# Performance work log

Measured on AMD Instinct MI355X. Metric: run time of the kernel, lower is better.

## Reference

```python
import jax, jax.numpy as jnp
import numpy as np

B, H, S, D = 1, 8, 4096, 64


def setup_inputs() -> dict:
    key = jax.random.key(0)
    kq, kk, kv = jax.random.split(key, 3)
    Q = jax.random.normal(kq, (B, H, S, D), dtype=jnp.float32)
    K = jax.random.normal(kk, (B, H, S, D), dtype=jnp.float32)
    V = jax.random.normal(kv, (B, H, S, D), dtype=jnp.float32)
    # causal mask: 1 where attention allowed, 0 where blocked (matches masked_fill(mask==0, -inf))
    mask = jnp.tril(jnp.ones((S, S), dtype=jnp.int32))[None, None, :, :]
    return {"Q": Q, "K": K, "V": V, "mask": mask}


def reference(Q, K, V, mask):
    d_k = Q.shape[-1]
    scale = 1.0 / jnp.sqrt(jnp.asarray(d_k, Q.dtype))
    # [B,H,S,S] attention scores
    attn_score = jnp.einsum("bhqd,bhkd->bhqk", Q, K) * scale
    neg_inf = jnp.asarray(-jnp.inf, attn_score.dtype)
    attn_score = jnp.where(mask == 0, neg_inf, attn_score)
    attn_weight = jax.nn.softmax(attn_score, axis=-1)
    attn_output = jnp.einsum("bhqk,bhkd->bhqd", attn_weight, V)
    return attn_output
```

## Files before the change

### kernel.cpp

```cpp
#include <hip/hip_runtime.h>

#define S_LEN 4096
#define NHEAD 8
#define DDIM  64
#define NT    64
#define TILE_BYTES 8192
#define WS_NEEDED (2ull * NHEAD * NT * TILE_BYTES)

typedef __attribute__((ext_vector_type(4))) float f32x4;
typedef __attribute__((ext_vector_type(2))) float f32x2;
typedef __attribute__((ext_vector_type(8))) short bf16x8;

__device__ __forceinline__ unsigned cvt_pk(float lo, float hi) {
  unsigned r;
  asm("v_cvt_pk_bf16_f32 %0, %1, %2" : "=v"(r) : "v"(lo), "v"(hi));
  return r;
}
__device__ __forceinline__ float ex2(float x) {
  float r;
  asm("v_exp_f32 %0, %1" : "=v"(r) : "v"(x));
  return r;
}
__device__ __forceinline__ unsigned short f2bf(float f) {
  unsigned u = __float_as_uint(f);
  return (unsigned short)((u + 0x7fffu + ((u >> 16) & 1u)) >> 16);
}
__device__ __forceinline__ unsigned pk2(float a, float b) {
  return (unsigned)f2bf(a) | ((unsigned)f2bf(b) << 16);
}

__global__ __launch_bounds__(256)
void prepass(const float* __restrict__ K, const float* __restrict__ V,
             char* __restrict__ wsK, char* __restrict__ wsV) {
  const int bid = blockIdx.x;
  const int h = bid & 7, t = bid >> 3;
  const int tid = threadIdx.x;
  const size_t base = ((size_t)h * S_LEN + t * 64) * DDIM;
  char* ck = wsK + (size_t)(h * NT + t) * TILE_BYTES;
  char* cv = wsV + (size_t)(h * NT + t) * TILE_BYTES;
  {
    const int key = tid >> 2;
    const int fn = key >> 4, lq = key & 15;
#pragma unroll
    for (int p = 0; p < 2; ++p) {
      const int du = (tid & 3) + p * 4;
      const int kk = du >> 2, g = du & 3;
      const float* src = K + base + (size_t)key * DDIM + du * 8;
      f32x4 a = *(const f32x4*)src;
      f32x4 b = *(const f32x4*)(src + 4);
      uint4 u = {cvt_pk(a[0], a[1]), cvt_pk(a[2], a[3]),
                 cvt_pk(b[0], b[1]), cvt_pk(b[2], b[3])};
      *(uint4*)(ck + kk * 4096 + fn * 1024 + g * 256 + lq * 16) = u;
    }
  }
  {
    const int kgrp = tid >> 5;
    const int d0 = (tid & 31) * 2;
    const int kk = kgrp >> 2, g = kgrp & 3;
    float va[8], vb[8];
#pragma unroll
    for (int jj = 0; jj < 8; ++jj) {
      f32x2 x = *(const f32x2*)(V + base + (size_t)(kgrp * 8 + jj) * DDIM + d0);
      va[jj] = x[0]; vb[jj] = x[1];
    }
    uint4 ua = {cvt_pk(va[0], va[1]), cvt_pk(va[2], va[3]),
                cvt_pk(va[4], va[5]), cvt_pk(va[6], va[7])};
    uint4 ub = {cvt_pk(vb[0], vb[1]), cvt_pk(vb[2], vb[3]),
                cvt_pk(vb[4], vb[5]), cvt_pk(vb[6], vb[7])};
    const int fm0 = d0 >> 4, lq0 = d0 & 15;
    const int fm1 = (d0 + 1) >> 4, lq1 = (d0 + 1) & 15;
    *(uint4*)(cv + kk * 4096 + fm0 * 1024 + g * 256 + lq0 * 16) = ua;
    *(uint4*)(cv + kk * 4096 + fm1 * 1024 + g * 256 + lq1 * 16) = ub;
  }
}

__global__ __launch_bounds__(256)
void attn_fwd13(const float* __restrict__ Q, const char* __restrict__ wsK,
                const char* __restrict__ wsV, float* __restrict__ O) {
  __shared__ __align__(16) char pool[25344];

  const int tid = threadIdx.x, wave = tid >> 6, lane = tid & 63;
  const int g = lane >> 4, lq = lane & 15;
  const int bid = blockIdx.x, h = bid & 7, i = bid >> 3;
  const int qc = 127 - i;
  const int jd = qc >> 1;
  const int qbase = qc * 32;
  const int n = (jd >= wave) ? ((jd - wave) >> 2) + 1 : 0;

  const char* tK = wsK + (size_t)h * NT * TILE_BYTES;
  const char* tV = wsV + (size_t)h * NT * TILE_BYTES;
  const int foff = lane * 16;

  const float qsc = 0.125f * 1.44269504088896340736f;
  bf16x8 qf[2][2];
#pragma unroll
  for (int qh = 0; qh < 2; ++qh) {
    const float* qp = Q + ((size_t)h * S_LEN + qbase + qh * 16 + lq) * DDIM + g * 8;
#pragma unroll
    for (int kk = 0; kk < 2; ++kk) {
      f32x4 a = *(const f32x4*)(qp + kk * 32);
      f32x4 b = *(const f32x4*)(qp + kk * 32 + 4);
      uint4 u = {cvt_pk(a[0] * qsc, a[1] * qsc), cvt_pk(a[2] * qsc, a[3] * qsc),
                 cvt_pk(b[0] * qsc, b[1] * qsc), cvt_pk(b[2] * qsc, b[3] * qsc)};
      qf[qh][kk] = __builtin_bit_cast(bf16x8, u);
    }
  }

  f32x4 of0[4], of1[4];
#pragma unroll
  for (int fm = 0; fm < 4; ++fm) { of0[fm] = (f32x4){0,0,0,0}; of1[fm] = (f32x4){0,0,0,0}; }
  float l0 = 0.f, l1 = 0.f;

  char* pbase = pool + wave * 4608;
  const int prow = lq * 72;

  bf16x8 kf[4][2], vf[4][2];
  f32x4 s0[4], s1[4];

  if (n > 0) {
    const char* pk = tK + (size_t)wave * TILE_BYTES + foff;
    const char* pv = tV + (size_t)wave * TILE_BYTES + foff;
#pragma unroll
    for (int fn = 0; fn < 4; ++fn)
#pragma unroll
      for (int kk = 0; kk < 2; ++kk) {
        kf[fn][kk] = *(const bf16x8*)(pk + kk * 4096 + fn * 1024);
        vf[fn][kk] = *(const bf16x8*)(pv + kk * 4096 + fn * 1024);
      }
#pragma unroll
    for (int fn = 0; fn < 4; ++fn) {
      f32x4 a = (f32x4){0,0,0,0}, b = (f32x4){0,0,0,0};
      a = __builtin_amdgcn_mfma_f32_16x16x32_bf16(kf[fn][0], qf[0][0], a, 0, 0, 0);
      a = __builtin_amdgcn_mfma_f32_16x16x32_bf16(kf[fn][1], qf[0][1], a, 0, 0, 0);
      b = __builtin_amdgcn_mfma_f32_16x16x32_bf16(kf[fn][0], qf[1][0], b, 0, 0, 0);
      b = __builtin_amdgcn_mfma_f32_16x16x32_bf16(kf[fn][1], qf[1][1], b, 0, 0, 0);
      s0[fn] = a; s1[fn] = b;
    }
    if (n > 1) {
      const char* pk2 = tK + (size_t)(wave + 4) * TILE_BYTES + foff;
#pragma unroll
      for (int fn = 0; fn < 4; ++fn)
#pragma unroll
        for (int kk = 0; kk < 2; ++kk)
          kf[fn][kk] = *(const bf16x8*)(pk2 + kk * 4096 + fn * 1024);
    }
  }

  int j = wave;
  for (int it = 0; it < n; ++it, j += 4) {

    if (j == jd) {
      const int koff = qbase - jd * 64;
#pragma unroll
      for (int fn = 0; fn < 4; ++fn)
#pragma unroll
        for (int rr = 0; rr < 4; ++rr) {
          const int key = fn * 16 + g * 4 + rr;
          if (key > koff + lq)      s0[fn][rr] = -__builtin_inff();
          if (key > koff + 16 + lq) s1[fn][rr] = -__builtin_inff();
        }
    }

    float rs0 = 0.f, rs1 = 0.f;
#pragma unroll
    for (int fn = 0; fn < 4; ++fn) {
      float a00 = ex2(s0[fn][0]), a01 = ex2(s0[fn][1]);
      float a02 = ex2(s0[fn][2]), a03 = ex2(s0[fn][3]);
      float a10 = ex2(s1[fn][0]), a11 = ex2(s1[fn][1]);
      float a12 = ex2(s1[fn][2]), a13 = ex2(s1[fn][3]);
      rs0 += (a00 + a01) + (a02 + a03);
      rs1 += (a10 + a11) + (a12 + a13);
      const int kk = fn >> 1;
      const int boff = ((fn & 1) * 2 + (g >> 1)) * 16 + (g & 1) * 8;
      unsigned long long w0 = (unsigned long long)cvt_pk(a00, a01)
                            | ((unsigned long long)cvt_pk(a02, a03) << 32);
      unsigned long long w1 = (unsigned long long)cvt_pk(a10, a11)
                            | ((unsigned long long)cvt_pk(a12, a13) << 32);
      *(unsigned long long*)(pbase + (kk * 2 + 0) * 1152 + prow + boff) = w0;
      *(unsigned long long*)(pbase + (kk * 2 + 1) * 1152 + prow + boff) = w1;
    }
    l0 += rs0; l1 += rs1;

    if (it + 1 < n) {
#pragma unroll
      for (int fn = 0; fn < 4; ++fn) {
        f32x4 a = (f32x4){0,0,0,0}, b = (f32x4){0,0,0,0};
        a = __builtin_amdgcn_mfma_f32_16x16x32_bf16(kf[fn][0], qf[0][0], a, 0, 0, 0);
        a = __builtin_amdgcn_mfma_f32_16x16x32_bf16(kf[fn][1], qf[0][1], a, 0, 0, 0);
        b = __builtin_amdgcn_mfma_f32_16x16x32_bf16(kf[fn][0], qf[1][0], b, 0, 0, 0);
        b = __builtin_amdgcn_mfma_f32_16x16x32_bf16(kf[fn][1], qf[1][1], b, 0, 0, 0);
        s0[fn] = a; s1[fn] = b;
      }
    }

    asm volatile("s_waitcnt lgkmcnt(0)" ::: "memory");

#pragma unroll
    for (int kk = 0; kk < 2; ++kk) {
      bf16x8 p0 = *(const bf16x8*)(pbase + (kk * 2 + 0) * 1152 + prow + g * 16);
      bf16x8 p1 = *(const bf16x8*)(pbase + (kk * 2 + 1) * 1152 + prow + g * 16);
#pragma unroll
      for (int fm = 0; fm < 4; ++fm) {
        of0[fm] = __builtin_amdgcn_mfma_f32_16x16x32_bf16(vf[fm][kk], p0, of0[fm], 0, 0, 0);
        of1[fm] = __builtin_amdgcn_mfma_f32_16x16x32_bf16(vf[fm][kk], p1, of1[fm], 0, 0, 0);
      }
    }

    if (it + 1 < n) {
      const char* pv = tV + (size_t)(j + 4) * TILE_BYTES + foff;
#pragma unroll
      for (int fm = 0; fm < 4; ++fm)
#pragma unroll
        for (int kk = 0; kk < 2; ++kk)
          vf[fm][kk] = *(const bf16x8*)(pv + kk * 4096 + fm * 1024);
      if (it + 2 < n) {
        const char* pk = tK + (size_t)(j + 8) * TILE_BYTES + foff;
#pragma unroll
        for (int fn = 0; fn < 4; ++fn)
#pragma unroll
          for (int kk = 0; kk < 2; ++kk)
            kf[fn][kk] = *(const bf16x8*)(pk + kk * 4096 + fn * 1024);
      }
    }
  }

  l0 += __shfl_xor(l0, 16); l0 += __shfl_xor(l0, 32);
  l1 += __shfl_xor(l1, 16); l1 += __shfl_xor(l1, 32);

  __syncthreads();
  if (wave < 3) {
    char* mb = pool + wave * 8192;
#pragma unroll
    for (int fm = 0; fm < 4; ++fm) {
      *(f32x4*)(mb + (fm * 2 + 0) * 1024 + g * 256 + lq * 16) = of0[fm];
      *(f32x4*)(mb + (fm * 2 + 1) * 1024 + g * 256 + lq * 16) = of1[fm];
    }
    if (g == 0) {
      f32x4 v = {l0, l1, 0.f, 0.f};
      *(f32x4*)(pool + 24576 + wave * 256 + lq * 16) = v;
    }
  }
  __syncthreads();
  if (wave == 3) {
    float den0 = l0, den1 = l1;
#pragma unroll
    for (int a = 0; a < 3; ++a) {
      f32x4 ml = *(const f32x4*)(pool + 24576 + a * 256 + lq * 16);
      den0 += ml[0];
      den1 += ml[1];
    }
    const float inv0 = 1.f / den0, inv1 = 1.f / den1;
    float* o0 = O + ((size_t)h * S_LEN + qbase + lq) * DDIM + g * 4;
    float* o1 = o0 + 16 * DDIM;
#pragma unroll
    for (int fm = 0; fm < 4; ++fm) {
      f32x4 r0 = of0[fm], r1 = of1[fm];
#pragma unroll
      for (int a = 0; a < 3; ++a) {
        r0 += *(const f32x4*)(pool + a * 8192 + (fm * 2 + 0) * 1024 + g * 256 + lq * 16);
        r1 += *(const f32x4*)(pool + a * 8192 + (fm * 2 + 1) * 1024 + g * 256 + lq * 16);
      }
      *(f32x4*)(o0 + fm * 16) = r0 * inv0;
      *(f32x4*)(o1 + fm * 16) = r1 * inv1;
    }
  }
}

__global__ __launch_bounds__(256, 2)
void attn_fwd_v1(const float* __restrict__ Q, const float* __restrict__ K,
                 const float* __restrict__ V, float* __restrict__ O) {
  __shared__ __align__(16) char kl[64 * 128];
  __shared__ __align__(16) char vt[64 * 128];
  __shared__ __align__(16) char pl[4 * 16 * 128];
  const int tid = threadIdx.x, wave = tid >> 6, lane = tid & 63;
  const int g = lane >> 4, lq = lane & 15;
  const int bid = blockIdx.x, h = bid & 7, i = bid >> 3;
  const int qt = (i & 1) ? (63 - (i >> 1)) : (i >> 1);
  const int qw = qt * 64 + wave * 16 + lq;
  const float* Qh = Q + ((size_t)h * S_LEN + qw) * DDIM;
  const float* Kh = K + (size_t)h * S_LEN * DDIM;
  const float* Vh = V + (size_t)h * S_LEN * DDIM;
  bf16x8 qf[2];
#pragma unroll
  for (int kk = 0; kk < 2; ++kk) {
    const float* p = Qh + g * 8 + kk * 32;
    f32x4 a = *(const f32x4*)p;
    f32x4 b = *(const f32x4*)(p + 4);
#pragma unroll
    for (int jj = 0; jj < 4; ++jj) {
      qf[kk][jj]     = (short)f2bf(a[jj] * 0.125f);
      qf[kk][jj + 4] = (short)f2bf(b[jj] * 0.125f);
    }
  }
  f32x4 of[4];
#pragma unroll
  for (int fm = 0; fm < 4; ++fm) of[fm] = (f32x4){0.f, 0.f, 0.f, 0.f};
  float mrun = -__builtin_inff(), lrun = 0.f;
  const int r16 = tid >> 4, c4 = tid & 15;
  const int vc = tid & 63, vkb = (tid >> 6) * 4;
  for (int j = 0; j <= qt; ++j) {
    const int k0 = j * 64;
    __syncthreads();
#pragma unroll
    for (int p = 0; p < 4; ++p) {
      const int rr = p * 16 + r16;
      f32x4 x = *(const f32x4*)(Kh + (size_t)(k0 + rr) * DDIM + c4 * 4);
      unsigned long long w = (unsigned long long)pk2(x[0], x[1])
                           | ((unsigned long long)pk2(x[2], x[3]) << 32);
      *(unsigned long long*)(kl + rr * 128 + ((c4 * 8) ^ ((rr & 7) << 4))) = w;
    }
#pragma unroll
    for (int p = 0; p < 4; ++p) {
      const int key = vkb + p * 16;
      const float* vp = Vh + (size_t)(k0 + key) * DDIM + vc;
      float v0 = vp[0], v1 = vp[DDIM], v2 = vp[2 * DDIM], v3 = vp[3 * DDIM];
      unsigned long long w = (unsigned long long)pk2(v0, v1)
                           | ((unsigned long long)pk2(v2, v3) << 32);
      *(unsigned long long*)(vt + vc * 128 + ((key * 2) ^ ((vc & 7) << 4))) = w;
    }
    __syncthreads();
    f32x4 sf[4];
#pragma unroll
    for (int fn = 0; fn < 4; ++fn) {
      f32x4 sv = (f32x4){0.f, 0.f, 0.f, 0.f};
#pragma unroll
      for (int kk = 0; kk < 2; ++kk) {
        const int krow = fn * 16 + lq;
        bf16x8 a = *(const bf16x8*)(kl + krow * 128 +
                                    ((g * 16 + kk * 64) ^ ((krow & 7) << 4)));
        sv = __builtin_amdgcn_mfma_f32_16x16x32_bf16(a, qf[kk], sv, 0, 0, 0);
      }
      sf[fn] = sv;
    }
    if (j == qt) {
      const int qrel = wave * 16 + lq;
#pragma unroll
      for (int fn = 0; fn < 4; ++fn)
#pragma unroll
        for (int rr = 0; rr < 4; ++rr)
          if (fn * 16 + g * 4 + rr > qrel) sf[fn][rr] = -__builtin_inff();
    }
    float mt = -__builtin_inff();
#pragma unroll
    for (int fn = 0; fn < 4; ++fn)
#pragma unroll
      for (int rr = 0; rr < 4; ++rr) mt = fmaxf(mt, sf[fn][rr]);
    mt = fmaxf(mt, __shfl_xor(mt, 16));
    mt = fmaxf(mt, __shfl_xor(mt, 32));
    const float mnew = fmaxf(mrun, mt);
    const float alpha = __expf(mrun - mnew);
    float rs = 0.f;
#pragma unroll
    for (int fn = 0; fn < 4; ++fn)
#pragma unroll
      for (int rr = 0; rr < 4; ++rr) {
        float p = __expf(sf[fn][rr] - mnew);
        sf[fn][rr] = p;
        rs += p;
      }
    rs += __shfl_xor(rs, 16);
    rs += __shfl_xor(rs, 32);
    mrun = mnew;
    lrun = lrun * alpha + rs;
#pragma unroll
    for (int fm = 0; fm < 4; ++fm) of[fm] *= alpha;
#pragma unroll
    for (int fn = 0; fn < 4; ++fn) {
      unsigned long long w = (unsigned long long)pk2(sf[fn][0], sf[fn][1])
                           | ((unsigned long long)pk2(sf[fn][2], sf[fn][3]) << 32);
      *(unsigned long long*)(pl + wave * 2048 + lq * 128 +
                             ((fn * 32 + g * 8) ^ ((lq & 7) << 4))) = w;
    }
    asm volatile("s_waitcnt lgkmcnt(0)" ::: "memory");
#pragma unroll
    for (int fm = 0; fm < 4; ++fm) {
#pragma unroll
      for (int kk = 0; kk < 2; ++kk) {
        const int vrow = fm * 16 + lq;
        bf16x8 av = *(const bf16x8*)(vt + vrow * 128 +
                                     ((g * 16 + kk * 64) ^ ((vrow & 7) << 4)));
        bf16x8 bp = *(const bf16x8*)(pl + wave * 2048 + lq * 128 +
                                     ((g * 16 + kk * 64) ^ ((lq & 7) << 4)));
        of[fm] = __builtin_amdgcn_mfma_f32_16x16x32_bf16(av, bp, of[fm], 0, 0, 0);
      }
    }
  }
  const float inv = 1.0f / lrun;
  float* orow = O + ((size_t)h * S_LEN + qw) * DDIM;
#pragma unroll
  for (int fm = 0; fm < 4; ++fm) {
    f32x4 o = of[fm] * inv;
    *(f32x4*)(orow + fm * 16 + g * 4) = o;
  }
}

extern "C" void kernel_launch(void* const* d_in, const int* in_sizes, int n_in,
                              void* d_out, int out_size, void* d_ws, size_t ws_size,
                              hipStream_t stream) {
  (void)in_sizes; (void)n_in; (void)out_size;
  const float* Q = (const float*)d_in[0];
  const float* K = (const float*)d_in[1];
  const float* V = (const float*)d_in[2];
  float* O = (float*)d_out;
  if (ws_size >= WS_NEEDED) {
    char* wsK = (char*)d_ws;
    char* wsV = wsK + (size_t)NHEAD * NT * TILE_BYTES;
    prepass<<<dim3(512), dim3(256), 0, stream>>>(K, V, wsK, wsV);
    attn_fwd13<<<dim3(1024), dim3(256), 0, stream>>>(Q, wsK, wsV, O);
  } else {
    attn_fwd_v1<<<dim3(512), dim3(256), 0, stream>>>(Q, K, V, O);
  }
}
```

Measured before the change: 43.30 us.

## Pair light and heavy causal query chunks in one 512-thread block

Each block now has 8 waves in two groups of four. One group handles query chunk p and the other handles chunk 127-p, so every block gets a short and a long causal row range and the per-block work is balanced. The grid is halved to 512 blocks of 512 threads, and shared memory doubles so each group has its own partial-sum merge area. This targets tail imbalance from uneven causal work across blocks, at the cost of larger blocks that may limit how many fit per CU.

```diff
diff --git a/kernel.cpp b/kernel.cpp
--- a/kernel.cpp
+++ b/kernel.cpp
@@ -74,24 +74,29 @@
   }
 }
 
-__global__ __launch_bounds__(256)
-void attn_fwd13(const float* __restrict__ Q, const char* __restrict__ wsK,
+__global__ __launch_bounds__(512)
+void attn_fwd18(const float* __restrict__ Q, const char* __restrict__ wsK,
                 const char* __restrict__ wsV, float* __restrict__ O) {
-  __shared__ __align__(16) char pool[25344];
+  __shared__ __align__(16) char pool[50688];
 
   const int tid = threadIdx.x, wave = tid >> 6, lane = tid & 63;
   const int g = lane >> 4, lq = lane & 15;
-  const int bid = blockIdx.x, h = bid & 7, i = bid >> 3;
-  const int qc = 127 - i;
+  const int w4 = wave & 3;
+  const int cg = wave >> 2;
+  const int bid = blockIdx.x, h = bid & 7, p = bid >> 3;
+
+  const int qc = cg ? (127 - p) : p;
   const int jd = qc >> 1;
   const int qbase = qc * 32;
-  const int n = (jd >= wave) ? ((jd - wave) >> 2) + 1 : 0;
+  const int n = (jd >= w4) ? ((jd - w4) >> 2) + 1 : 0;
 
   const char* tK = wsK + (size_t)h * NT * TILE_BYTES;
   const char* tV = wsV + (size_t)h * NT * TILE_BYTES;
   const int foff = lane * 16;
-
   const float qsc = 0.125f * 1.44269504088896340736f;
+  char* pbase = pool + wave * 4608;
+  const int prow = lq * 72;
+
   bf16x8 qf[2][2];
 #pragma unroll
   for (int qh = 0; qh < 2; ++qh) {
@@ -111,15 +116,12 @@
   for (int fm = 0; fm < 4; ++fm) { of0[fm] = (f32x4){0,0,0,0}; of1[fm] = (f32x4){0,0,0,0}; }
   float l0 = 0.f, l1 = 0.f;
 
-  char* pbase = pool + wave * 4608;
-  const int prow = lq * 72;
-
   bf16x8 kf[4][2], vf[4][2];
   f32x4 s0[4], s1[4];
 
   if (n > 0) {
-    const char* pk = tK + (size_t)wave * TILE_BYTES + foff;
-    const char* pv = tV + (size_t)wave * TILE_BYTES + foff;
+    const char* pk = tK + (size_t)w4 * TILE_BYTES + foff;
+    const char* pv = tV + (size_t)w4 * TILE_BYTES + foff;
 #pragma unroll
     for (int fn = 0; fn < 4; ++fn)
 #pragma unroll
@@ -137,7 +139,7 @@
       s0[fn] = a; s1[fn] = b;
     }
     if (n > 1) {
-      const char* pk2 = tK + (size_t)(wave + 4) * TILE_BYTES + foff;
+      const char* pk2 = tK + (size_t)(w4 + 4) * TILE_BYTES + foff;
 #pragma unroll
       for (int fn = 0; fn < 4; ++fn)
 #pragma unroll
@@ -146,9 +148,8 @@
     }
   }
 
-  int j = wave;
+  int j = w4;
   for (int it = 0; it < n; ++it, j += 4) {
-
     if (j == jd) {
       const int koff = qbase - jd * 64;
 #pragma unroll
@@ -228,8 +229,9 @@
   l1 += __shfl_xor(l1, 16); l1 += __shfl_xor(l1, 32);
 
   __syncthreads();
-  if (wave < 3) {
-    char* mb = pool + wave * 8192;
+  char* mpool = pool + cg * 25344;
+  if (w4 < 3) {
+    char* mb = mpool + w4 * 8192;
 #pragma unroll
     for (int fm = 0; fm < 4; ++fm) {
       *(f32x4*)(mb + (fm * 2 + 0) * 1024 + g * 256 + lq * 16) = of0[fm];
@@ -237,15 +239,15 @@
     }
     if (g == 0) {
       f32x4 v = {l0, l1, 0.f, 0.f};
-      *(f32x4*)(pool + 24576 + wave * 256 + lq * 16) = v;
+      *(f32x4*)(mpool + 24576 + w4 * 256 + lq * 16) = v;
     }
   }
   __syncthreads();
-  if (wave == 3) {
+  if (w4 == 3) {
     float den0 = l0, den1 = l1;
 #pragma unroll
     for (int a = 0; a < 3; ++a) {
-      f32x4 ml = *(const f32x4*)(pool + 24576 + a * 256 + lq * 16);
+      f32x4 ml = *(const f32x4*)(mpool + 24576 + a * 256 + lq * 16);
       den0 += ml[0];
       den1 += ml[1];
     }
@@ -257,8 +259,8 @@
       f32x4 r0 = of0[fm], r1 = of1[fm];
 #pragma unroll
       for (int a = 0; a < 3; ++a) {
-        r0 += *(const f32x4*)(pool + a * 8192 + (fm * 2 + 0) * 1024 + g * 256 + lq * 16);
-        r1 += *(const f32x4*)(pool + a * 8192 + (fm * 2 + 1) * 1024 + g * 256 + lq * 16);
+        r0 += *(const f32x4*)(mpool + a * 8192 + (fm * 2 + 0) * 1024 + g * 256 + lq * 16);
+        r1 += *(const f32x4*)(mpool + a * 8192 + (fm * 2 + 1) * 1024 + g * 256 + lq * 16);
       }
       *(f32x4*)(o0 + fm * 16) = r0 * inv0;
       *(f32x4*)(o1 + fm * 16) = r1 * inv1;
@@ -406,7 +408,7 @@
     char* wsK = (char*)d_ws;
     char* wsV = wsK + (size_t)NHEAD * NT * TILE_BYTES;
     prepass<<<dim3(512), dim3(256), 0, stream>>>(K, V, wsK, wsV);
-    attn_fwd13<<<dim3(1024), dim3(256), 0, stream>>>(Q, wsK, wsV, O);
+    attn_fwd18<<<dim3(512), dim3(512), 0, stream>>>(Q, wsK, wsV, O);
   } else {
     attn_fwd_v1<<<dim3(512), dim3(256), 0, stream>>>(Q, K, V, O);
   }
```

New measurement: 43.62 us. No clear change (+0.7%).
